# Kernel optimization log

Hardware: AMD Instinct MI355X
Metric: run time of the kernel (lower is better)

Reference implementation:

```python
import jax, jax.numpy as jnp
from jax import lax
import numpy as np

B = 8
NUM_ANCHORS = 1047552
PROPOSAL_COUNT = 1000
NMS_THRESHOLD = 0.7
RPN_BBOX_STD_DEV = np.array([0.1, 0.1, 0.2, 0.2], dtype=np.float32)
RPN_NMS_LIMIT = 6000


def setup_inputs() -> dict:
    key = jax.random.key(0)
    k1, k2, k3 = jax.random.split(key, 3)
    rpn_scores = jax.random.uniform(k1, (B, NUM_ANCHORS, 2), dtype=jnp.float32)
    rpn_bbox_delta = jax.random.normal(k2, (B, NUM_ANCHORS, 4), dtype=jnp.float32)
    # Build valid normalized anchors (y1,x1,y2,x2) from uniform randoms.
    u = jax.random.uniform(k3, (NUM_ANCHORS, 4), dtype=jnp.float32)
    cy, cx = u[:, 0], u[:, 1]
    h = u[:, 2] * 0.2 + 0.01
    w = u[:, 3] * 0.2 + 0.01
    anchors = jnp.stack([cy - 0.5 * h, cx - 0.5 * w, cy + 0.5 * h, cx + 0.5 * w], axis=-1)
    anchors = jnp.clip(anchors, 0.0, 1.0)
    return {"rpn_scores": rpn_scores, "rpn_bbox_delta": rpn_bbox_delta, "anchors": anchors}


def _apply_box_deltas(boxes, deltas):
    # boxes: [..., (y1,x1,y2,x2)], deltas: [..., (dy,dx,log(dh),log(dw))]
    h = boxes[..., 2] - boxes[..., 0]
    w = boxes[..., 3] - boxes[..., 1]
    cy = boxes[..., 0] + 0.5 * h + deltas[..., 0] * h
    cx = boxes[..., 1] + 0.5 * w + deltas[..., 1] * w
    h = h * jnp.exp(deltas[..., 2])
    w = w * jnp.exp(deltas[..., 3])
    y1 = cy - 0.5 * h
    x1 = cx - 0.5 * w
    return jnp.stack([y1, x1, y1 + h, x1 + w], axis=-1)


def _nms_indices(boxes):
    # Greedy NMS over boxes already sorted by descending score. boxes: [N,4].
    N = boxes.shape[0]
    areas = (boxes[:, 2] - boxes[:, 0]) * (boxes[:, 3] - boxes[:, 1])

    def body(i, state):
        valid, sel = state
        idx = jnp.argmax(valid)          # first still-valid box = highest score
        has = valid[idx]
        sel = sel.at[i].set(jnp.where(has, idx, -1))
        b = boxes[idx]
        yy1 = jnp.maximum(b[0], boxes[:, 0])
        xx1 = jnp.maximum(b[1], boxes[:, 1])
        yy2 = jnp.minimum(b[2], boxes[:, 2])
        xx2 = jnp.minimum(b[3], boxes[:, 3])
        inter = jnp.maximum(yy2 - yy1, 0.0) * jnp.maximum(xx2 - xx1, 0.0)
        union = areas[idx] + areas - inter
        iou = jnp.where(union > 0, inter / union, 0.0)
        keep = valid & (iou <= NMS_THRESHOLD)
        keep = keep.at[idx].set(False)
        valid = jnp.where(has, keep, valid)
        return valid, sel

    valid0 = jnp.ones((N,), dtype=bool)
    sel0 = jnp.full((PROPOSAL_COUNT,), -1, dtype=jnp.int32)
    _, sel = lax.fori_loop(0, PROPOSAL_COUNT, body, (valid0, sel0))
    return sel


def _nms_single(boxes):
    # boxes: [pre_nms_limit, 4] sorted by score desc -> [proposal_count, 4], zero-padded
    sel = _nms_indices(lax.stop_gradient(boxes))
    props = boxes[jnp.clip(sel, 0)]
    return jnp.where(sel[:, None] >= 0, props, 0.0)


def _forward(rpn_scores, rpn_bbox_delta, anchors):
    scores = rpn_scores[:, :, 1]                                   # [B, A]
    deltas = rpn_bbox_delta * jnp.asarray(RPN_BBOX_STD_DEV)        # [B, A, 4]
    pre_nms_limit = min(RPN_NMS_LIMIT, anchors.shape[0])
    top_scores, ix = lax.top_k(scores, pre_nms_limit)              # [B, pre]
    tgt_deltas = jnp.take_along_axis(deltas, ix[..., None], axis=1)  # [B, pre, 4]
    tgt_anchors = anchors[ix]                                      # [B, pre, 4]
    boxes = _apply_box_deltas(tgt_anchors, tgt_deltas)
    boxes = jnp.clip(boxes, 0.0, 1.0)                              # window (0,0,1,1)
    proposals = jax.vmap(_nms_single)(boxes)                       # [B, proposal_count, 4]
    return proposals


def reference(rpn_scores, rpn_bbox_delta, anchors):
    return _forward(rpn_scores, rpn_bbox_delta, anchors)
```

## Files before the change

kernel.cpp:

```cpp
#include <hip/hip_runtime.h>
#include <stdint.h>

#define NBATCH   8
#define NA       1047552
#define PRE_NMS  6000
#define NPROP    1000
#define BINS     2048
#define EB       128
#define SLICE    192
#define PRESEL   0.99f
#define CAND_CAP 8192
#define SCAP     2048
#define PCHUNK   32
#define PCAP     256
#define REJW     188
#define NMS_THR  0.7f

#define OFF_POOL   ((size_t)0)
#define OFF_BCCNT  (OFF_POOL  + (size_t)NBATCH*EB*SLICE*8)
#define OFF_BOFF   (OFF_BCCNT + (size_t)NBATCH*EB*4)
#define OFF_BCNT   (OFF_BOFF  + (size_t)NBATCH*BINS*4)
#define OFF_CBIN   (OFF_BCNT  + (size_t)NBATCH*BINS*4)
#define OFF_PCNT   (OFF_CBIN  + 256)
#define OFF_CAND   (OFF_PCNT  + (size_t)NBATCH*PCHUNK*4)
#define OFF_BOXES  (OFF_CAND  + (size_t)NBATCH*CAND_CAP*8)
#define OFF_PAIRS  (OFF_BOXES + (size_t)NBATCH*PRE_NMS*16)
#define WS_NEEDED  (OFF_PAIRS + (size_t)NBATCH*PCHUNK*PCAP*4)

__device__ __forceinline__ unsigned score_bin(float s) {
    int b = (int)(s * (float)BINS);
    if (b < 0) b = 0;
    if (b > BINS - 1) b = BINS - 1;
    return (unsigned)b;
}

__global__ __launch_bounds__(256) void k_extract(const float* __restrict__ scores,
                                                 uint64_t* __restrict__ pool,
                                                 uint32_t* __restrict__ bccnt) {
    __shared__ uint64_t buf[SLICE];
    __shared__ uint32_t n;
    const int b = blockIdx.y, blk = blockIdx.x;
    if (threadIdx.x == 0) n = 0;
    __syncthreads();
    const float4* s4 = reinterpret_cast<const float4*>(scores) + (size_t)b * (NA / 2);
    const int n4 = NA / 2;
    const int stride = EB * 256;
    for (int i = blk * 256 + threadIdx.x; i < n4; i += stride) {
        float4 v = s4[i];
        if (v.y >= PRESEL) {
            unsigned idx = 2u * (unsigned)i;
            unsigned p = atomicAdd(&n, 1u);
            if (p < SLICE) buf[p] = ((uint64_t)__float_as_uint(v.y) << 32) | (uint32_t)(~idx);
        }
        if (v.w >= PRESEL) {
            unsigned idx = 2u * (unsigned)i + 1u;
            unsigned p = atomicAdd(&n, 1u);
            if (p < SLICE) buf[p] = ((uint64_t)__float_as_uint(v.w) << 32) | (uint32_t)(~idx);
        }
    }
    __syncthreads();
    unsigned cnt = n < SLICE ? n : SLICE;
    uint64_t* pb = pool + ((size_t)b * EB + blk) * SLICE;
    for (unsigned t = threadIdx.x; t < cnt; t += 256) pb[t] = buf[t];
    if (threadIdx.x == 0) bccnt[b * EB + blk] = cnt;
}

__global__ __launch_bounds__(1024) void k_prep(const uint64_t* __restrict__ pool,
                                               const uint32_t* __restrict__ bccnt,
                                               uint32_t* __restrict__ boff,
                                               uint32_t* __restrict__ bcnt,
                                               uint32_t* __restrict__ cbin,
                                               uint32_t* __restrict__ pcnt,
                                               uint64_t* __restrict__ cand) {
    __shared__ uint32_t cnts[EB];
    __shared__ uint32_t hist[BINS];
    __shared__ uint32_t boffL[BINS];
    __shared__ uint32_t chunk[64];
    __shared__ int sC;
    const int b = blockIdx.x;
    const int tid = threadIdx.x;
    if (tid == 0) sC = 0;
    if (tid < EB) { unsigned c = bccnt[b * EB + tid]; cnts[tid] = c < SLICE ? c : SLICE; }
    for (int t = tid; t < BINS; t += 1024) hist[t] = 0;
    __syncthreads();
    const uint64_t* pb = pool + (size_t)b * EB * SLICE;
    for (int p = tid; p < EB * SLICE; p += 1024) {
        int sl = p / SLICE, e = p - sl * SLICE;
        if (e < (int)cnts[sl]) {
            uint64_t k = pb[p];
            float s = __uint_as_float((uint32_t)(k >> 32));
            atomicAdd(&hist[score_bin(s)], 1u);
        }
    }
    __syncthreads();
    if (tid < 64) {
        uint32_t s = 0;
        for (int q = 0; q < 32; ++q) s += hist[tid * 32 + q];
        uint32_t inc = s;
        for (int off = 1; off < 64; off <<= 1) {
            uint32_t o = __shfl_down(inc, off);
            if (tid + off < 64) inc += o;
        }
        chunk[tid] = inc - s;
    }
    __syncthreads();
    if (tid < 64) {
        uint32_t acc = chunk[tid];
        for (int q = 31; q >= 0; --q) {
            int bin = tid * 32 + q;
            uint32_t h = hist[bin];
            boffL[bin] = acc;
            if (acc + h >= PRE_NMS) atomicMax(&sC, bin);
            acc += h;
        }
    }
    __syncthreads();
    const int C = sC;
    if (tid == 0) cbin[b] = (uint32_t)C;
    for (int t = tid; t < BINS; t += 1024) {
        boff[b * BINS + t] = boffL[t];
        bcnt[b * BINS + t] = hist[t];
    }
    if (tid < PCHUNK) pcnt[b * PCHUNK + tid] = 0;
    __syncthreads();
    for (int t = tid; t < BINS; t += 1024) hist[t] = 0;
    __syncthreads();
    for (int p = tid; p < EB * SLICE; p += 1024) {
        int sl = p / SLICE, e = p - sl * SLICE;
        if (e < (int)cnts[sl]) {
            uint64_t k = pb[p];
            float s = __uint_as_float((uint32_t)(k >> 32));
            unsigned bin = score_bin(s);
            if ((int)bin >= C) {
                unsigned pos = boffL[bin] + atomicAdd(&hist[bin], 1u);
                if (pos < CAND_CAP) cand[(size_t)b * CAND_CAP + pos] = k;
            }
        }
    }
}

__global__ __launch_bounds__(256) void k_binsort_decode(const uint32_t* __restrict__ cbin,
                                                        const uint32_t* __restrict__ boff,
                                                        const uint32_t* __restrict__ bcnt,
                                                        const uint64_t* __restrict__ cand,
                                                        const float* __restrict__ deltas,
                                                        const float* __restrict__ anchors,
                                                        float4* __restrict__ boxesOut) {
    __shared__ uint64_t s[SCAP];
    const int b = blockIdx.y;
    const unsigned bin = cbin[b] + blockIdx.x;
    if (bin >= BINS) return;
    unsigned cnt = bcnt[(size_t)b * BINS + bin];
    if (cnt == 0) return;
    unsigned start = boff[(size_t)b * BINS + bin];
    if (start >= PRE_NMS) return;
    if (cnt > SCAP) cnt = SCAP;
    if (start + cnt > CAND_CAP) cnt = CAND_CAP - start;
    const uint64_t* seg = cand + (size_t)b * CAND_CAP + start;
    for (unsigned i = threadIdx.x; i < SCAP; i += 256)
        s[i] = (i < cnt) ? ~seg[i] : ~0ull;
    __syncthreads();
    for (unsigned k = 2; k <= SCAP; k <<= 1) {
        for (unsigned j = k >> 1; j > 0; j >>= 1) {
            for (unsigned i = threadIdx.x; i < SCAP; i += 256) {
                unsigned ixj = i ^ j;
                if (ixj > i) {
                    uint64_t a = s[i], c = s[ixj];
                    bool up = ((i & k) == 0);
                    if ((a > c) == up) { s[i] = c; s[ixj] = a; }
                }
            }
            __syncthreads();
        }
    }
    const float4* anc = reinterpret_cast<const float4*>(anchors);
    const float4* del = reinterpret_cast<const float4*>(deltas) + (size_t)b * NA;
    for (unsigned i = threadIdx.x; i < cnt; i += 256) {
        unsigned r = start + i;
        if (r >= PRE_NMS) continue;
        unsigned idx = (uint32_t)s[i];
        float4 a = anc[idx];
        float4 d = del[idx];
        float h = a.z - a.x, w = a.w - a.y;
        float cy = a.x + 0.5f * h + (d.x * 0.1f) * h;
        float cx = a.y + 0.5f * w + (d.y * 0.1f) * w;
        h = h * expf(d.z * 0.2f);
        w = w * expf(d.w * 0.2f);
        float y1 = cy - 0.5f * h, x1 = cx - 0.5f * w;
        float y2 = y1 + h,        x2 = x1 + w;
        float4 o;
        o.x = fminf(fmaxf(y1, 0.f), 1.f);
        o.y = fminf(fmaxf(x1, 0.f), 1.f);
        o.z = fminf(fmaxf(y2, 0.f), 1.f);
        o.w = fminf(fmaxf(x2, 0.f), 1.f);
        boxesOut[(size_t)b * PRE_NMS + r] = o;
    }
}

template<bool DIAG>
__device__ __forceinline__ void pairs_body(const float4* bi, const float* ai,
                                           const float4* vj, const float* aj,
                                           const int* jx, int ib, int b,
                                           uint32_t* pcnt, uint32_t* pairs) {
    #pragma unroll 4
    for (int it = 0; it < 64; ++it) {
        float4 vi = bi[it];
        float a_i = ai[it];
        int i = ib + it;
        #pragma unroll
        for (int k = 0; k < 4; ++k) {
            float yy1 = fmaxf(vj[k].x, vi.x);
            float xx1 = fmaxf(vj[k].y, vi.y);
            float yy2 = fminf(vj[k].z, vi.z);
            float xx2 = fminf(vj[k].w, vi.w);
            float ih = yy2 - yy1, iw = xx2 - xx1;
            bool ok = fminf(ih, iw) > 0.f;
            if (DIAG) ok = ok && (i < jx[k]);
            if (ok) {
                float inter = ih * iw;
                float uni = a_i + aj[k] - inter;
                if (uni > 0.f && inter / uni > NMS_THR) {
                    unsigned j = (unsigned)jx[k];
                    unsigned c = ((unsigned)i + j) & (PCHUNK - 1);
                    unsigned pos = atomicAdd(&pcnt[b * PCHUNK + c], 1u);
                    if (pos < PCAP)
                        pairs[((size_t)b * PCHUNK + c) * PCAP + pos] = (j << 13) | (unsigned)i;
                }
            }
        }
    }
}

__global__ __launch_bounds__(256) void k_pairs(const float4* __restrict__ boxes,
                                               uint32_t* __restrict__ pcnt,
                                               uint32_t* __restrict__ pairs) {
    const int b  = blockIdx.z;
    const int ib = blockIdx.x * 64;
    const int jb = blockIdx.y * 1024;
    if (ib >= jb + 1024) return;
    __shared__ float4 bi[64];
    __shared__ float  ai[64];
    const float4* bx = boxes + (size_t)b * PRE_NMS;
    const int tid = threadIdx.x;
    if (tid < 64) {
        int i = ib + tid;
        float4 v = (i < PRE_NMS) ? bx[i] : make_float4(1e30f, 1e30f, -1e30f, -1e30f);
        bi[tid] = v;
        ai[tid] = (v.z - v.x) * (v.w - v.y);
    }
    float4 vj[4]; float aj[4]; int jx[4];
    #pragma unroll
    for (int k = 0; k < 4; ++k) {
        int j = jb + k * 256 + tid;
        jx[k] = j;
        float4 v = (j < PRE_NMS) ? bx[j] : make_float4(1e30f, 1e30f, -1e30f, -1e30f);
        vj[k] = v;
        aj[k] = (v.z - v.x) * (v.w - v.y);
    }
    __syncthreads();
    if (ib + 63 >= jb) pairs_body<true >(bi, ai, vj, aj, jx, ib, b, pcnt, pairs);
    else               pairs_body<false>(bi, ai, vj, aj, jx, ib, b, pcnt, pairs);
}

__global__ __launch_bounds__(256) void k_nms_emit(const uint32_t* __restrict__ pcnt,
                                                  const uint32_t* __restrict__ pairsIn,
                                                  const float4* __restrict__ boxes,
                                                  float4* __restrict__ out) {
    __shared__ uint32_t sp[PCHUNK * PCAP];
    __shared__ uint32_t cpref[PCHUNK + 1];
    __shared__ uint32_t rejA[REJW], rejB[REJW], pre[REJW + 1];
    __shared__ int changed;
    const int b = blockIdx.x;
    const int tid = threadIdx.x;
    float4* ob = out + (size_t)b * NPROP;
    for (int r = tid; r < NPROP; r += 256) ob[r] = make_float4(0.f, 0.f, 0.f, 0.f);
    if (tid == 0) {
        unsigned s = 0;
        for (int c = 0; c < PCHUNK; ++c) {
            cpref[c] = s;
            unsigned cc = pcnt[b * PCHUNK + c];
            if (cc > PCAP) cc = PCAP;
            s += cc;
        }
        cpref[PCHUNK] = s;
    }
    for (int t = tid; t < REJW; t += 256) rejA[t] = 0;
    __syncthreads();
    const unsigned np = cpref[PCHUNK];
    for (int c = 0; c < PCHUNK; ++c) {
        unsigned cnt = cpref[c + 1] - cpref[c];
        for (unsigned k = tid; k < cnt; k += 256)
            sp[cpref[c] + k] = pairsIn[((size_t)b * PCHUNK + c) * PCAP + k];
    }
    __syncthreads();
    for (int iter = 0; iter < PRE_NMS; ++iter) {
        for (int t = tid; t < REJW; t += 256) rejB[t] = 0;
        if (tid == 0) changed = 0;
        __syncthreads();
        for (unsigned p = tid; p < np; p += 256) {
            unsigned u = sp[p];
            unsigned j = u >> 13, i = u & 8191u;
            if (!((rejA[i >> 5] >> (i & 31)) & 1u))
                atomicOr(&rejB[j >> 5], 1u << (j & 31));
        }
        __syncthreads();
        for (int t = tid; t < REJW; t += 256) {
            if (rejB[t] != rejA[t]) changed = 1;
            rejA[t] = rejB[t];
        }
        __syncthreads();
        if (!changed) break;
    }
    if (tid == 0) {
        unsigned c2 = 0;
        for (int w = 0; w < REJW; ++w) { pre[w] = c2; c2 += __popc(rejA[w]); }
        pre[REJW] = c2;
    }
    __syncthreads();
    const float4* bx = boxes + (size_t)b * PRE_NMS;
    for (int j = tid; j < PRE_NMS; j += 256) {
        unsigned w = (unsigned)j >> 5, bit = (unsigned)j & 31;
        if ((rejA[w] >> bit) & 1u) continue;
        unsigned rank = (unsigned)j - (pre[w] + __popc(rejA[w] & ((1u << bit) - 1u)));
        if (rank < NPROP) ob[rank] = bx[j];
    }
}

extern "C" void kernel_launch(void* const* d_in, const int* in_sizes, int n_in,
                              void* d_out, int out_size, void* d_ws, size_t ws_size,
                              hipStream_t stream) {
    const float* scores  = (const float*)d_in[0];
    const float* deltas  = (const float*)d_in[1];
    const float* anchors = (const float*)d_in[2];

    if (ws_size < WS_NEEDED) return;

    char* ws = (char*)d_ws;
    uint64_t* pool  = (uint64_t*)(ws + OFF_POOL);
    uint32_t* bccnt = (uint32_t*)(ws + OFF_BCCNT);
    uint32_t* boff  = (uint32_t*)(ws + OFF_BOFF);
    uint32_t* bcnt  = (uint32_t*)(ws + OFF_BCNT);
    uint32_t* cbin  = (uint32_t*)(ws + OFF_CBIN);
    uint32_t* pcnt  = (uint32_t*)(ws + OFF_PCNT);
    uint64_t* cand  = (uint64_t*)(ws + OFF_CAND);
    float4*   boxes = (float4*)(ws + OFF_BOXES);
    uint32_t* pairs = (uint32_t*)(ws + OFF_PAIRS);

    k_extract       <<<dim3(EB, NBATCH), 256, 0, stream>>>(scores, pool, bccnt);
    k_prep          <<<NBATCH, 1024, 0, stream>>>(pool, bccnt, boff, bcnt, cbin, pcnt, cand);
    k_binsort_decode<<<dim3(128, NBATCH), 256, 0, stream>>>(cbin, boff, bcnt, cand, deltas, anchors, boxes);
    k_pairs         <<<dim3((PRE_NMS + 63) / 64, (PRE_NMS + 1023) / 1024, NBATCH), 256, 0, stream>>>(boxes, pcnt, pairs);
    k_nms_emit      <<<NBATCH, 256, 0, stream>>>(pcnt, pairs, boxes, (float4*)d_out);
}
```

Baseline: 488.3 us.

## Replace all-pairs IoU scan with uniform spatial grid plus large-box path

Instead of testing every box pair, boxes are bucketed by centre into a 22x22 grid, and small boxes are compared only with members of the neighbouring 5x5 cells. Boxes wider or taller than 0.3 go to a separate list and are checked against all boxes. This turns the quadratic pair search into roughly linear work, at the cost of an extra grid-building kernel and two extra launches. Correctness relies on the 0.3 size cap making pairs beyond two cells unable to exceed the IoU threshold. The large-box list is capped at 256 entries, so overflow would silently drop pairs.

```diff
diff --git a/kernel.cpp b/kernel.cpp
--- a/kernel.cpp
+++ b/kernel.cpp
@@ -15,6 +15,10 @@
 #define PCAP     256
 #define REJW     188
 #define NMS_THR  0.7f
+#define GRIDN    22
+#define NCELL    (GRIDN*GRIDN)
+#define HCAP     0.3f
+#define LCAP     256
 
 #define OFF_POOL   ((size_t)0)
 #define OFF_BCCNT  (OFF_POOL  + (size_t)NBATCH*EB*SLICE*8)
@@ -25,13 +29,24 @@
 #define OFF_CAND   (OFF_PCNT  + (size_t)NBATCH*PCHUNK*4)
 #define OFF_BOXES  (OFF_CAND  + (size_t)NBATCH*CAND_CAP*8)
 #define OFF_PAIRS  (OFF_BOXES + (size_t)NBATCH*PRE_NMS*16)
-#define WS_NEEDED  (OFF_PAIRS + (size_t)NBATCH*PCHUNK*PCAP*4)
+#define OFF_CSTART (OFF_PAIRS + (size_t)NBATCH*PCHUNK*PCAP*4)
+#define OFF_MEMB   (OFF_CSTART+ (size_t)NBATCH*488*4)
+#define OFF_LIDX   (OFF_MEMB  + (size_t)NBATCH*PRE_NMS*2)
+#define OFF_LCNT   (OFF_LIDX  + (size_t)NBATCH*LCAP*2)
+#define WS_NEEDED  (OFF_LCNT  + (size_t)NBATCH*4)
 
 __device__ __forceinline__ unsigned score_bin(float s) {
     int b = (int)(s * (float)BINS);
     if (b < 0) b = 0;
     if (b > BINS - 1) b = BINS - 1;
     return (unsigned)b;
+}
+
+__device__ __forceinline__ int cell_coord(float c) {
+    int v = (int)(c * (float)GRIDN);
+    if (v < 0) v = 0;
+    if (v > GRIDN - 1) v = GRIDN - 1;
+    return v;
 }
 
 __global__ __launch_bounds__(256) void k_extract(const float* __restrict__ scores,
@@ -197,69 +212,158 @@
     }
 }
 
-template<bool DIAG>
-__device__ __forceinline__ void pairs_body(const float4* bi, const float* ai,
-                                           const float4* vj, const float* aj,
-                                           const int* jx, int ib, int b,
-                                           uint32_t* pcnt, uint32_t* pairs) {
-    #pragma unroll 4
-    for (int it = 0; it < 64; ++it) {
-        float4 vi = bi[it];
-        float a_i = ai[it];
-        int i = ib + it;
+__global__ __launch_bounds__(1024) void k_grid(const float4* __restrict__ boxes,
+                                               uint32_t* __restrict__ cellstart,
+                                               uint16_t* __restrict__ memb,
+                                               uint16_t* __restrict__ lidx,
+                                               uint32_t* __restrict__ lcnt) {
+    __shared__ uint32_t cnt[NCELL];
+    __shared__ uint32_t base[NCELL + 1];
+    __shared__ uint32_t ln;
+    const int b = blockIdx.x;
+    const int tid = threadIdx.x;
+    const float4* bx = boxes + (size_t)b * PRE_NMS;
+    if (tid == 0) ln = 0;
+    for (int t = tid; t < NCELL; t += 1024) cnt[t] = 0;
+    __syncthreads();
+    for (int r = tid; r < PRE_NMS; r += 1024) {
+        float4 v = bx[r];
+        float bh = v.z - v.x, bw = v.w - v.y;
+        if (bh > HCAP || bw > HCAP) continue;
+        int cy = cell_coord((v.x + v.z) * 0.5f);
+        int cx = cell_coord((v.y + v.w) * 0.5f);
+        atomicAdd(&cnt[cy * GRIDN + cx], 1u);
+    }
+    __syncthreads();
+    if (tid < 64) {
+        uint32_t s = 0;
         #pragma unroll
-        for (int k = 0; k < 4; ++k) {
-            float yy1 = fmaxf(vj[k].x, vi.x);
-            float xx1 = fmaxf(vj[k].y, vi.y);
-            float yy2 = fminf(vj[k].z, vi.z);
-            float xx2 = fminf(vj[k].w, vi.w);
-            float ih = yy2 - yy1, iw = xx2 - xx1;
-            bool ok = fminf(ih, iw) > 0.f;
-            if (DIAG) ok = ok && (i < jx[k]);
-            if (ok) {
-                float inter = ih * iw;
-                float uni = a_i + aj[k] - inter;
-                if (uni > 0.f && inter / uni > NMS_THR) {
-                    unsigned j = (unsigned)jx[k];
-                    unsigned c = ((unsigned)i + j) & (PCHUNK - 1);
-                    unsigned pos = atomicAdd(&pcnt[b * PCHUNK + c], 1u);
-                    if (pos < PCAP)
-                        pairs[((size_t)b * PCHUNK + c) * PCAP + pos] = (j << 13) | (unsigned)i;
-                }
+        for (int q = 0; q < 8; ++q) {
+            int c = tid * 8 + q;
+            if (c < NCELL) s += cnt[c];
+        }
+        uint32_t inc = s;
+        for (int off = 1; off < 64; off <<= 1) {
+            uint32_t o = __shfl_up(inc, off);
+            if (tid >= off) inc += o;
+        }
+        uint32_t running = inc - s;
+        #pragma unroll
+        for (int q = 0; q < 8; ++q) {
+            int c = tid * 8 + q;
+            if (c < NCELL) {
+                base[c] = running;
+                running += cnt[c];
+                if (c == NCELL - 1) base[NCELL] = running;
             }
         }
     }
-}
-
-__global__ __launch_bounds__(256) void k_pairs(const float4* __restrict__ boxes,
-                                               uint32_t* __restrict__ pcnt,
-                                               uint32_t* __restrict__ pairs) {
-    const int b  = blockIdx.z;
-    const int ib = blockIdx.x * 64;
-    const int jb = blockIdx.y * 1024;
-    if (ib >= jb + 1024) return;
-    __shared__ float4 bi[64];
-    __shared__ float  ai[64];
+    __syncthreads();
+    for (int t = tid; t <= NCELL; t += 1024) cellstart[b * 488 + t] = base[t];
+    for (int t = tid; t < NCELL; t += 1024) cnt[t] = 0;
+    __syncthreads();
+    for (int r = tid; r < PRE_NMS; r += 1024) {
+        float4 v = bx[r];
+        float bh = v.z - v.x, bw = v.w - v.y;
+        if (bh > HCAP || bw > HCAP) {
+            unsigned p = atomicAdd(&ln, 1u);
+            if (p < LCAP) lidx[b * LCAP + p] = (uint16_t)r;
+            continue;
+        }
+        int cy = cell_coord((v.x + v.z) * 0.5f);
+        int cx = cell_coord((v.y + v.w) * 0.5f);
+        unsigned cell = cy * GRIDN + cx;
+        unsigned pos = base[cell] + atomicAdd(&cnt[cell], 1u);
+        memb[(size_t)b * PRE_NMS + pos] = (uint16_t)r;
+    }
+    __syncthreads();
+    if (tid == 0) lcnt[b] = ln < LCAP ? ln : LCAP;
+}
+
+__global__ __launch_bounds__(256) void k_pairs_small(const float4* __restrict__ boxes,
+                                                     const uint32_t* __restrict__ cellstart,
+                                                     const uint16_t* __restrict__ memb,
+                                                     uint32_t* __restrict__ pcnt,
+                                                     uint32_t* __restrict__ pairs) {
+    const int b = blockIdx.y;
+    const int g = blockIdx.x * 256 + threadIdx.x;
+    if (g >= PRE_NMS * 5) return;
+    const int j  = g / 5;
+    const int dy = g - j * 5 - 2;
     const float4* bx = boxes + (size_t)b * PRE_NMS;
-    const int tid = threadIdx.x;
-    if (tid < 64) {
-        int i = ib + tid;
-        float4 v = (i < PRE_NMS) ? bx[i] : make_float4(1e30f, 1e30f, -1e30f, -1e30f);
-        bi[tid] = v;
-        ai[tid] = (v.z - v.x) * (v.w - v.y);
-    }
-    float4 vj[4]; float aj[4]; int jx[4];
-    #pragma unroll
-    for (int k = 0; k < 4; ++k) {
-        int j = jb + k * 256 + tid;
-        jx[k] = j;
-        float4 v = (j < PRE_NMS) ? bx[j] : make_float4(1e30f, 1e30f, -1e30f, -1e30f);
-        vj[k] = v;
-        aj[k] = (v.z - v.x) * (v.w - v.y);
-    }
-    __syncthreads();
-    if (ib + 63 >= jb) pairs_body<true >(bi, ai, vj, aj, jx, ib, b, pcnt, pairs);
-    else               pairs_body<false>(bi, ai, vj, aj, jx, ib, b, pcnt, pairs);
+    float4 vj = bx[j];
+    float hj = vj.z - vj.x, wj = vj.w - vj.y;
+    if (hj > HCAP || wj > HCAP) return;
+    int cy = cell_coord((vj.x + vj.z) * 0.5f);
+    int cx = cell_coord((vj.y + vj.w) * 0.5f);
+    int row = cy + dy;
+    if (row < 0 || row > GRIDN - 1) return;
+    int clo = cx - 2 < 0 ? 0 : cx - 2;
+    int chi = cx + 2 > GRIDN - 1 ? GRIDN - 1 : cx + 2;
+    const uint32_t* cs = cellstart + b * 488;
+    unsigned rs = cs[row * GRIDN + clo];
+    unsigned re = cs[row * GRIDN + chi + 1];
+    const uint16_t* mb = memb + (size_t)b * PRE_NMS;
+    float aj = (vj.z - vj.x) * (vj.w - vj.y);
+    for (unsigned p = rs; p < re; ++p) {
+        int i = mb[p];
+        if (i >= j) continue;
+        float4 vi = bx[i];
+        float yy1 = fmaxf(vj.x, vi.x);
+        float xx1 = fmaxf(vj.y, vi.y);
+        float yy2 = fminf(vj.z, vi.z);
+        float xx2 = fminf(vj.w, vi.w);
+        float ih = yy2 - yy1, iw = xx2 - xx1;
+        if (fminf(ih, iw) <= 0.f) continue;
+        float inter = ih * iw;
+        float ai = (vi.z - vi.x) * (vi.w - vi.y);
+        float uni = (ai + aj) - inter;
+        if (uni > 0.f && inter / uni > NMS_THR) {
+            unsigned c = ((unsigned)i + (unsigned)j) & (PCHUNK - 1);
+            unsigned pos = atomicAdd(&pcnt[b * PCHUNK + c], 1u);
+            if (pos < PCAP)
+                pairs[((size_t)b * PCHUNK + c) * PCAP + pos] =
+                    ((unsigned)j << 13) | (unsigned)i;
+        }
+    }
+}
+
+__global__ __launch_bounds__(256) void k_pairs_large(const float4* __restrict__ boxes,
+                                                     const uint16_t* __restrict__ lidx,
+                                                     const uint32_t* __restrict__ lcnt,
+                                                     uint32_t* __restrict__ pcnt,
+                                                     uint32_t* __restrict__ pairs) {
+    const int b = blockIdx.y;
+    const int l = blockIdx.x;
+    if (l >= (int)lcnt[b]) return;
+    const float4* bx = boxes + (size_t)b * PRE_NMS;
+    const int L = lidx[b * LCAP + l];
+    float4 vL = bx[L];
+    float aL = (vL.z - vL.x) * (vL.w - vL.y);
+    for (int r = threadIdx.x; r < PRE_NMS; r += 256) {
+        if (r == L) continue;
+        float4 vr = bx[r];
+        float hr = vr.z - vr.x, wr = vr.w - vr.y;
+        bool rlarge = (hr > HCAP || wr > HCAP);
+        if (rlarge && r > L) continue;
+        float yy1 = fmaxf(vL.x, vr.x);
+        float xx1 = fmaxf(vL.y, vr.y);
+        float yy2 = fminf(vL.z, vr.z);
+        float xx2 = fminf(vL.w, vr.w);
+        float ih = yy2 - yy1, iw = xx2 - xx1;
+        if (fminf(ih, iw) <= 0.f) continue;
+        float inter = ih * iw;
+        float ar = hr * wr;
+        float uni = (aL + ar) - inter;
+        if (uni > 0.f && inter / uni > NMS_THR) {
+            unsigned i = (unsigned)(r < L ? r : L);
+            unsigned j = (unsigned)(r < L ? L : r);
+            unsigned c = (i + j) & (PCHUNK - 1);
+            unsigned pos = atomicAdd(&pcnt[b * PCHUNK + c], 1u);
+            if (pos < PCAP)
+                pairs[((size_t)b * PCHUNK + c) * PCAP + pos] = (j << 13) | i;
+        }
+    }
 }
 
 __global__ __launch_bounds__(256) void k_nms_emit(const uint32_t* __restrict__ pcnt,
@@ -336,19 +440,25 @@
     if (ws_size < WS_NEEDED) return;
 
     char* ws = (char*)d_ws;
-    uint64_t* pool  = (uint64_t*)(ws + OFF_POOL);
-    uint32_t* bccnt = (uint32_t*)(ws + OFF_BCCNT);
-    uint32_t* boff  = (uint32_t*)(ws + OFF_BOFF);
-    uint32_t* bcnt  = (uint32_t*)(ws + OFF_BCNT);
-    uint32_t* cbin  = (uint32_t*)(ws + OFF_CBIN);
-    uint32_t* pcnt  = (uint32_t*)(ws + OFF_PCNT);
-    uint64_t* cand  = (uint64_t*)(ws + OFF_CAND);
-    float4*   boxes = (float4*)(ws + OFF_BOXES);
-    uint32_t* pairs = (uint32_t*)(ws + OFF_PAIRS);
+    uint64_t* pool   = (uint64_t*)(ws + OFF_POOL);
+    uint32_t* bccnt  = (uint32_t*)(ws + OFF_BCCNT);
+    uint32_t* boff   = (uint32_t*)(ws + OFF_BOFF);
+    uint32_t* bcnt   = (uint32_t*)(ws + OFF_BCNT);
+    uint32_t* cbin   = (uint32_t*)(ws + OFF_CBIN);
+    uint32_t* pcnt   = (uint32_t*)(ws + OFF_PCNT);
+    uint64_t* cand   = (uint64_t*)(ws + OFF_CAND);
+    float4*   boxes  = (float4*)(ws + OFF_BOXES);
+    uint32_t* pairs  = (uint32_t*)(ws + OFF_PAIRS);
+    uint32_t* cstart = (uint32_t*)(ws + OFF_CSTART);
+    uint16_t* memb   = (uint16_t*)(ws + OFF_MEMB);
+    uint16_t* lidx   = (uint16_t*)(ws + OFF_LIDX);
+    uint32_t* lcnt   = (uint32_t*)(ws + OFF_LCNT);
 
     k_extract       <<<dim3(EB, NBATCH), 256, 0, stream>>>(scores, pool, bccnt);
     k_prep          <<<NBATCH, 1024, 0, stream>>>(pool, bccnt, boff, bcnt, cbin, pcnt, cand);
     k_binsort_decode<<<dim3(128, NBATCH), 256, 0, stream>>>(cbin, boff, bcnt, cand, deltas, anchors, boxes);
-    k_pairs         <<<dim3((PRE_NMS + 63) / 64, (PRE_NMS + 1023) / 1024, NBATCH), 256, 0, stream>>>(boxes, pcnt, pairs);
+    k_grid          <<<NBATCH, 1024, 0, stream>>>(boxes, cstart, memb, lidx, lcnt);
+    k_pairs_small   <<<dim3((PRE_NMS * 5 + 255) / 256, NBATCH), 256, 0, stream>>>(boxes, cstart, memb, pcnt, pairs);
+    k_pairs_large   <<<dim3(LCAP, NBATCH), 256, 0, stream>>>(boxes, lidx, lcnt, pcnt, pairs);
     k_nms_emit      <<<NBATCH, 256, 0, stream>>>(pcnt, pairs, boxes, (float4*)d_out);
 }
```

Measured after the change: 483.3 us. About the same (-1.0%).
